# Kernel optimization log

Hardware: AMD Instinct MI355X
Metric: run time of the kernel (lower is better)

## Reference

```python
import jax, jax.numpy as jnp
import numpy as np

B, N, M = 2, 2048, 1024
C, CTX, H = 1024, 1024, 16
D = C // H
HID = int(C * 4.0)
EPS = 1e-6


def _ln(h):
    # LayerNorm32: fp32 layernorm, eps=1e-6, no affine params
    h32 = h.astype(jnp.float32)
    mu = jnp.mean(h32, axis=-1, keepdims=True)
    var = jnp.var(h32, axis=-1, keepdims=True)
    return ((h32 - mu) * jax.lax.rsqrt(var + EPS)).astype(h.dtype)


def _sdpa(q, k, v):
    # q: [B,Q,H,D], k/v: [B,K,H,D]
    scale = 1.0 / np.sqrt(D)
    s = jnp.einsum('bqhd,bkhd->bhqk', q, k) * scale
    p = jax.nn.softmax(s, axis=-1)
    return jnp.einsum('bhqk,bkhd->bqhd', p, v)


def _forward(x, context, Wqkv, bqkv, Wos, bos, Wq, bq, Wkv, bkv, Woc, boc, W1, b1, W2, b2):
    Bx, Nx, _ = x.shape
    Mx = context.shape[1]
    # --- self-attention (attn_mode='full') ---
    h = _ln(x)
    qkv = (h @ Wqkv + bqkv).reshape(Bx, Nx, 3, H, D)
    q, k, v = qkv[:, :, 0], qkv[:, :, 1], qkv[:, :, 2]
    a = _sdpa(q, k, v).reshape(Bx, Nx, C)
    x = x + (a @ Wos + bos)
    # --- cross-attention (always 'full') ---
    h = _ln(x)
    q = (h @ Wq + bq).reshape(Bx, Nx, H, D)
    kv = (context @ Wkv + bkv).reshape(Bx, Mx, 2, H, D)
    k, v = kv[:, :, 0], kv[:, :, 1]
    a = _sdpa(q, k, v).reshape(Bx, Nx, C)
    x = x + (a @ Woc + boc)
    # --- FFN with tanh-approx GELU ---
    h = _ln(x)
    x = x + (jax.nn.gelu(h @ W1 + b1, approximate=True) @ W2 + b2)
    return x


def setup_inputs() -> dict:
    key = jax.random.key(0)
    ks = jax.random.split(key, 12)
    rn = lambda k, shape: (jax.random.normal(k, shape, jnp.float32) * 0.02)
    return {
        'x': jax.random.normal(ks[0], (B, N, C), jnp.float32),
        'context': jax.random.normal(ks[1], (B, M, CTX), jnp.float32),
        'Wqkv': rn(ks[2], (C, 3 * C)), 'bqkv': jnp.zeros((3 * C,), jnp.float32),
        'Wos': rn(ks[3], (C, C)), 'bos': jnp.zeros((C,), jnp.float32),
        'Wq': rn(ks[4], (C, C)), 'bq': jnp.zeros((C,), jnp.float32),
        'Wkv': rn(ks[5], (CTX, 2 * C)), 'bkv': jnp.zeros((2 * C,), jnp.float32),
        'Woc': rn(ks[6], (C, C)), 'boc': jnp.zeros((C,), jnp.float32),
        'W1': rn(ks[7], (C, HID)), 'b1': jnp.zeros((HID,), jnp.float32),
        'W2': rn(ks[8], (HID, C)), 'b2': jnp.zeros((C,), jnp.float32),
    }


def reference(x, context, Wqkv, bqkv, Wos, bos, Wq, bq, Wkv, bkv, Woc, boc, W1, b1, W2, b2):
    return _forward(x, context, Wqkv, bqkv, Wos, bos, Wq, bq, Wkv, bkv, Woc, boc, W1, b1, W2, b2)
```

## Files before the change

kernel.cpp:

```cpp
#include <hip/hip_runtime.h>
#include <cstdint>

typedef unsigned short u16;
typedef short bf16x8 __attribute__((ext_vector_type(8)));
typedef unsigned short u16x8 __attribute__((ext_vector_type(8)));
typedef float f32x4 __attribute__((ext_vector_type(4)));

__device__ __forceinline__ u16 f2bf(float f) {
  union { float f; uint32_t u; } v; v.f = f;
  uint32_t r = (v.u + 0x7fffu + ((v.u >> 16) & 1u)) >> 16;
  return (u16)r;
}

__device__ __forceinline__ void gload_lds16(const u16* g, u16* l) {
  __builtin_amdgcn_global_load_lds(
      (const __attribute__((address_space(1))) void*)g,
      (__attribute__((address_space(3))) void*)l, 16, 0, 0);
}

__device__ __forceinline__ void ln_body(const float* __restrict__ x,
                                        u16* __restrict__ h, int row) {
  const int tid = threadIdx.x;
  const float4 v = *reinterpret_cast<const float4*>(x + (long)row * 1024 + tid * 4);
  float s  = v.x + v.y + v.z + v.w;
  float ss = v.x * v.x + v.y * v.y + v.z * v.z + v.w * v.w;
#pragma unroll
  for (int off = 32; off >= 1; off >>= 1) {
    s  += __shfl_xor(s, off, 64);
    ss += __shfl_xor(ss, off, 64);
  }
  __shared__ float red[8];
  const int wave = tid >> 6, lane = tid & 63;
  if (lane == 0) { red[wave] = s; red[4 + wave] = ss; }
  __syncthreads();
  s  = red[0] + red[1] + red[2] + red[3];
  ss = red[4] + red[5] + red[6] + red[7];
  const float mu   = s * (1.0f / 1024.0f);
  const float var  = ss * (1.0f / 1024.0f) - mu * mu;
  const float rstd = rsqrtf(var + 1e-6f);
  ushort4 o;
  o.x = f2bf((v.x - mu) * rstd);
  o.y = f2bf((v.y - mu) * rstd);
  o.z = f2bf((v.z - mu) * rstd);
  o.w = f2bf((v.w - mu) * rstd);
  *reinterpret_cast<ushort4*>(h + (long)row * 1024 + tid * 4) = o;
}

__global__ __launch_bounds__(256) void ln_kernel(const float* __restrict__ x,
                                                 u16* __restrict__ h) {
  ln_body(x, h, blockIdx.x);
}

struct WEnt { const float* W; u16* Wt; int K, N, tEnd; };
struct WEnts { WEnt e[4]; int n; };

__device__ __forceinline__ void wconv_body(const WEnts& args, int t) {
  __shared__ u16 tile[64][72];
  int i = 0, tStart = 0;
  while (i < args.n - 1 && t >= args.e[i].tEnd) { tStart = args.e[i].tEnd; i++; }
  const float* W = args.e[i].W;
  u16* Wt = args.e[i].Wt;
  const int K = args.e[i].K, N = args.e[i].N;
  const int rel = t - tStart;
  const int ntn = N >> 6;
  const int tn = rel % ntn, tk = rel / ntn;
  const int n0 = tn * 64, k0 = tk * 64;

  const int th = threadIdx.x;
  const int c4 = (th & 15) * 4;
  const int r  = th >> 4;
#pragma unroll
  for (int ii = 0; ii < 4; ii++) {
    const int row = ii * 16 + r;
    const float4 v = *reinterpret_cast<const float4*>(W + (long)(k0 + row) * N + n0 + c4);
    tile[c4 + 0][row] = f2bf(v.x);
    tile[c4 + 1][row] = f2bf(v.y);
    tile[c4 + 2][row] = f2bf(v.z);
    tile[c4 + 3][row] = f2bf(v.w);
  }
  __syncthreads();
  const int c8 = (th & 7) * 8;
  const int rn = th >> 3;
#pragma unroll
  for (int ii = 0; ii < 2; ii++) {
    const int row = ii * 32 + rn;
    *reinterpret_cast<u16x8*>(Wt + (long)(n0 + row) * K + k0 + c8) =
        *reinterpret_cast<const u16x8*>(&tile[row][c8]);
  }
}

__global__ __launch_bounds__(256) void wconvert_all(WEnts args) {
  wconv_body(args, blockIdx.x);
}

__global__ __launch_bounds__(256) void ln_wconv_combo(const float* __restrict__ x,
                                                      u16* __restrict__ h, int nLn,
                                                      WEnts args) {
  if ((int)blockIdx.x < nLn) ln_body(x, h, blockIdx.x);
  else                       wconv_body(args, blockIdx.x - nLn);
}

__global__ __launch_bounds__(256) void wconv_f2bf_combo(WEnts args, int nW,
                                                        const float* __restrict__ in,
                                                        u16* __restrict__ out) {
  if ((int)blockIdx.x < nW) {
    wconv_body(args, blockIdx.x);
  } else {
    const long i = ((long)(blockIdx.x - nW) * 256 + threadIdx.x) * 4;
    const float4 v = *reinterpret_cast<const float4*>(in + i);
    ushort4 o;
    o.x = f2bf(v.x); o.y = f2bf(v.y); o.z = f2bf(v.z); o.w = f2bf(v.w);
    *reinterpret_cast<ushort4*>(out + i) = o;
  }
}

__global__ __launch_bounds__(256) void vtrans(const u16* __restrict__ V,
                                              u16* __restrict__ Vt,
                                              int vStride, long vBatch, int nk) {
  __shared__ u16 tile[64][72];
  const int t = threadIdx.x;
  const int b = blockIdx.z, h = blockIdx.y, n0 = blockIdx.x * 64;
  const u16* vp = V + (long)b * vBatch + h * 64;
  u16* op = Vt + (long)(b * 16 + h) * 64 * (long)nk + n0;
  const int ch = t & 7;
#pragma unroll
  for (int i = 0; i < 2; i++) {
    const int n = (t >> 3) + i * 32;
    const u16x8 v = *reinterpret_cast<const u16x8*>(vp + (long)(n0 + n) * vStride + ch * 8);
#pragma unroll
    for (int j = 0; j < 8; j++) tile[ch * 8 + j][n] = v[j];
  }
  __syncthreads();
#pragma unroll
  for (int i = 0; i < 2; i++) {
    const int d = (t >> 3) + i * 32;
    *reinterpret_cast<u16x8*>(op + (long)d * nk + ch * 8) =
        *reinterpret_cast<const u16x8*>(&tile[d][ch * 8]);
  }
}

template <int TN, bool OUT_BF16, bool GELU_ACT, bool RES>
__device__ __forceinline__ void gemm_core(
    const u16* __restrict__ A, const u16* __restrict__ Bt,
    const float* __restrict__ bias, const float* __restrict__ res,
    void* __restrict__ Cout, int Ndim, int Kdim, int m0, int n0,
    u16* Al, u16* Bl) {
  constexpr int NFRAG = TN / 32;
  const int tid  = threadIdx.x;
  const int lane = tid & 63, wave = tid >> 6;
  const int quad = lane >> 4, l15 = lane & 15;
  const int wr = wave >> 1, wc = wave & 1;

  f32x4 acc[4][NFRAG];
  const f32x4 vzero = {0.f, 0.f, 0.f, 0.f};
#pragma unroll
  for (int i = 0; i < 4; i++)
#pragma unroll
    for (int jj = 0; jj < NFRAG; jj++) acc[i][jj] = vzero;

  const long rowOff = (long)(lane >> 2) * Kdim + (((lane & 3) ^ ((lane >> 3) & 3)) * 8);
  const u16* gA = A  + (long)m0 * Kdim + rowOff;
  const u16* gB = Bt + (long)n0 * Kdim + rowOff;

  auto stage = [&](int k0, int p) {
    gload_lds16(gA + (long)(wave * 16) * Kdim + k0,       Al + p * 4096 + wave * 512);
    gload_lds16(gA + (long)((wave + 4) * 16) * Kdim + k0, Al + p * 4096 + (wave + 4) * 512);
    gload_lds16(gB + (long)(wave * 16) * Kdim + k0,       Bl + p * (TN * 32) + wave * 512);
    if constexpr (TN == 128)
      gload_lds16(gB + (long)((wave + 4) * 16) * Kdim + k0, Bl + p * (TN * 32) + (wave + 4) * 512);
  };

  const int swz = (quad ^ ((l15 >> 1) & 3)) * 8;

  stage(0, 0);
  int p = 0;
  for (int k0 = 0; k0 < Kdim; k0 += 32, p ^= 1) {
    __syncthreads();
    bf16x8 af[4], bfr[NFRAG];
#pragma unroll
    for (int mt = 0; mt < 4; mt++)
      af[mt] = *reinterpret_cast<const bf16x8*>(Al + p * 4096 + (wr * 64 + mt * 16 + l15) * 32 + swz);
#pragma unroll
    for (int nt = 0; nt < NFRAG; nt++)
      bfr[nt] = *reinterpret_cast<const bf16x8*>(Bl + p * (TN * 32) + (wc * NFRAG * 16 + nt * 16 + l15) * 32 + swz);
    if (k0 + 32 < Kdim) stage(k0 + 32, p ^ 1);
#pragma unroll
    for (int mt = 0; mt < 4; mt++)
#pragma unroll
      for (int nt = 0; nt < NFRAG; nt++)
        acc[mt][nt] = __builtin_amdgcn_mfma_f32_16x16x32_bf16(af[mt], bfr[nt], acc[mt][nt], 0, 0, 0);
  }

#pragma unroll
  for (int nt = 0; nt < NFRAG; nt++) {
    const int col = n0 + wc * NFRAG * 16 + nt * 16 + l15;
    const float bv = bias[col];
#pragma unroll
    for (int mt = 0; mt < 4; mt++) {
#pragma unroll
      for (int r = 0; r < 4; r++) {
        const int row = m0 + wr * 64 + mt * 16 + quad * 4 + r;
        float y = acc[mt][nt][r] + bv;
        if (GELU_ACT) {
          const float t = 0.7978845608028654f * (y + 0.044715f * y * y * y);
          y = y / (1.0f + __builtin_amdgcn_exp2f(-2.885390081777927f * t));
        }
        if (RES) y += res[(long)row * Ndim + col];
        if (OUT_BF16)
          ((u16*)Cout)[(long)row * Ndim + col] = f2bf(y);
        else
          ((float*)Cout)[(long)row * Ndim + col] = y;
      }
    }
  }
}

template <int TN, int SX, bool OUT_BF16, bool GELU_ACT, bool RES>
__global__ __launch_bounds__(256, 2) void gemm_bt(
    const u16* __restrict__ A, const u16* __restrict__ Bt,
    const float* __restrict__ bias, const float* __restrict__ res,
    void* __restrict__ Cout, int Ndim, int Kdim, int lx, int ly) {
  __shared__ u16 Al[2 * 128 * 32];
  __shared__ u16 Bl[2 * TN * 32];
  const int j = blockIdx.x;
  const int c = j & 7, kk = j >> 3;
  const int cx = c % SX, cy = c / SX;
  const int bx = cx * lx + (kk % lx);
  const int by = cy * ly + (kk / lx);
  gemm_core<TN, OUT_BF16, GELU_ACT, RES>(
      A, Bt, bias, res, Cout, Ndim, Kdim, by * 128, bx * TN, Al, Bl);
}

struct GemmSeg {
  const u16* A; const u16* Bt; const float* bias; u16* C;
  int Ndim, Kdim, SX, lx, ly;
};
struct GemmDualP { GemmSeg s0, s1; int nBlk0; };

template <int TN>
__global__ __launch_bounds__(256, 2) void gemm_dual(GemmDualP pp) {
  __shared__ u16 Al[2 * 128 * 32];
  __shared__ u16 Bl[2 * TN * 32];
  int j = blockIdx.x;
  GemmSeg s;
  if (j < pp.nBlk0) { s = pp.s0; } else { s = pp.s1; j -= pp.nBlk0; }
  const int c = j & 7, kk = j >> 3;
  const int cx = c % s.SX, cy = c / s.SX;
  const int bx = cx * s.lx + (kk % s.lx);
  const int by = cy * s.ly + (kk / s.lx);
  gemm_core<TN, true, false, false>(
      s.A, s.Bt, s.bias, nullptr, s.C, s.Ndim, s.Kdim, by * 128, bx * TN, Al, Bl);
}

__global__ __launch_bounds__(256, 2) void attn_kernel(
    const u16* __restrict__ Q, const u16* __restrict__ K, const u16* __restrict__ Vt,
    u16* __restrict__ O, int nk, int qStride, int kStride, int oStride,
    long qBatch, long kBatch, long oBatch) {
  __shared__ u16 Kt[2][64 * 64];
  __shared__ u16 Vl[2][64 * 64];
  __shared__ u16 Pl[4][32 * 64];

  const int tid = threadIdx.x;
  const int lane = tid & 63, wave = tid >> 6;
  const int quad = lane >> 4, l15 = lane & 15;
  const int b = blockIdx.z, hh = blockIdx.y, qt = blockIdx.x;

  const u16* qp = Q + (long)b * qBatch + hh * 64;
  const u16* kp = K + (long)b * kBatch + hh * 64;
  const u16* vp = Vt + (long)(b * 16 + hh) * 64 * (long)nk;

  bf16x8 qf[2][2];
  const int qrow = qt * 128 + wave * 32 + l15;
#pragma unroll
  for (int qg = 0; qg < 2; qg++) {
    qf[qg][0] = *reinterpret_cast<const bf16x8*>(qp + (long)(qrow + qg * 16) * qStride + quad * 8);
    qf[qg][1] = *reinterpret_cast<const bf16x8*>(qp + (long)(qrow + qg * 16) * qStride + 32 + quad * 8);
  }

  const int r8 = lane >> 3;
  const int gcol = ((lane & 7) ^ r8) * 8;
  const u16* kgA = kp + (long)(wave * 8 + r8) * kStride + gcol;
  const u16* kgB = kp + (long)((wave + 4) * 8 + r8) * kStride + gcol;
  const u16* vgA = vp + (long)(wave * 8 + r8) * nk + gcol;
  const u16* vgB = vp + (long)((wave + 4) * 8 + r8) * nk + gcol;

  const int cF = (quad ^ (l15 & 7)) * 8;

  const f32x4 vzero = {0.f, 0.f, 0.f, 0.f};
  f32x4 oAcc[2][4];
  float lSt[2] = {0.f, 0.f};
#pragma unroll
  for (int qg = 0; qg < 2; qg++)
#pragma unroll
    for (int i = 0; i < 4; i++) oAcc[qg][i] = vzero;

  const float SCL = 0.18033688f;
  const int nTiles = nk >> 6;
  const long kAdv = (long)64 * kStride;

  auto stage = [&](int kt, int p) {
    gload_lds16(kgA + kt * kAdv, &Kt[p][wave * 512]);
    gload_lds16(kgB + kt * kAdv, &Kt[p][(wave + 4) * 512]);
    gload_lds16(vgA + kt * 64,   &Vl[p][wave * 512]);
    gload_lds16(vgB + kt * 64,   &Vl[p][(wave + 4) * 512]);
  };

  stage(0, 0);
  int p = 0;
  for (int kt = 0; kt < nTiles; kt++, p ^= 1) {
    __syncthreads();
    if (kt + 1 < nTiles) stage(kt + 1, p ^ 1);

    f32x4 st[2][4];
#pragma unroll
    for (int mt = 0; mt < 4; mt++) {
      const bf16x8 kf0 = *reinterpret_cast<const bf16x8*>(&Kt[p][(mt * 16 + l15) * 64 + cF]);
      const bf16x8 kf1 = *reinterpret_cast<const bf16x8*>(&Kt[p][(mt * 16 + l15) * 64 + (cF ^ 32)]);
#pragma unroll
      for (int qg = 0; qg < 2; qg++) {
        f32x4 z = vzero;
        z = __builtin_amdgcn_mfma_f32_16x16x32_bf16(kf0, qf[qg][0], z, 0, 0, 0);
        z = __builtin_amdgcn_mfma_f32_16x16x32_bf16(kf1, qf[qg][1], z, 0, 0, 0);
        st[qg][mt] = z;
      }
    }

#pragma unroll
    for (int qg = 0; qg < 2; qg++) {
      float ps = 0.f;
#pragma unroll
      for (int mt = 0; mt < 4; mt++)
#pragma unroll
        for (int r = 0; r < 4; r++) {
          const float pw = __builtin_amdgcn_exp2f(st[qg][mt][r] * SCL);
          st[qg][mt][r] = pw;
          ps += pw;
        }
      lSt[qg] += ps;
      u16* plw = &Pl[wave][(qg * 16 + l15) * 64];
#pragma unroll
      for (int mt = 0; mt < 4; mt++) {
        union { float f; uint32_t u; } a0, a1, a2, a3;
        a0.f = st[qg][mt][0]; a1.f = st[qg][mt][1];
        a2.f = st[qg][mt][2]; a3.f = st[qg][mt][3];
        a0.u += 0x8000u; a1.u += 0x8000u; a2.u += 0x8000u; a3.u += 0x8000u;
        uint2 w;
        w.x = __builtin_amdgcn_perm(a1.u, a0.u, 0x07060302u);
        w.y = __builtin_amdgcn_perm(a3.u, a2.u, 0x07060302u);
        const int pcol = (((mt * 2 + (quad >> 1)) ^ (l15 & 7)) * 8) + (quad & 1) * 4;
        *reinterpret_cast<uint2*>(&plw[pcol]) = w;
      }
    }

    bf16x8 pf[2][2];
#pragma unroll
    for (int qg = 0; qg < 2; qg++) {
      const u16* plw = &Pl[wave][(qg * 16 + l15) * 64];
      pf[qg][0] = *reinterpret_cast<const bf16x8*>(&plw[cF]);
      pf[qg][1] = *reinterpret_cast<const bf16x8*>(&plw[cF ^ 32]);
    }
#pragma unroll
    for (int dt = 0; dt < 4; dt++) {
      const bf16x8 vf0 = *reinterpret_cast<const bf16x8*>(&Vl[p][(dt * 16 + l15) * 64 + cF]);
      const bf16x8 vf1 = *reinterpret_cast<const bf16x8*>(&Vl[p][(dt * 16 + l15) * 64 + (cF ^ 32)]);
#pragma unroll
      for (int qg = 0; qg < 2; qg++) {
        oAcc[qg][dt] = __builtin_amdgcn_mfma_f32_16x16x32_bf16(pf[qg][0], vf0, oAcc[qg][dt], 0, 0, 0);
        oAcc[qg][dt] = __builtin_amdgcn_mfma_f32_16x16x32_bf16(pf[qg][1], vf1, oAcc[qg][dt], 0, 0, 0);
      }
    }
  }

  u16* op = O + (long)b * oBatch + hh * 64;
#pragma unroll
  for (int qg = 0; qg < 2; qg++) {
    float l = lSt[qg];
    l += __shfl_xor(l, 16, 64);
    l += __shfl_xor(l, 32, 64);
    float lR[4];
#pragma unroll
    for (int r = 0; r < 4; r++) lR[r] = 1.0f / __shfl(l, quad * 4 + r, 64);
#pragma unroll
    for (int dt = 0; dt < 4; dt++)
#pragma unroll
      for (int r = 0; r < 4; r++) {
        const int row = qt * 128 + wave * 32 + qg * 16 + quad * 4 + r;
        op[(long)row * oStride + dt * 16 + l15] = f2bf(oAcc[qg][dt][r] * lR[r]);
      }
  }
}

extern "C" void kernel_launch(void* const* d_in, const int* in_sizes, int n_in,
                              void* d_out, int out_size, void* d_ws, size_t ws_size,
                              hipStream_t stream) {
  const float* x    = (const float*)d_in[0];
  const float* ctx  = (const float*)d_in[1];
  const float* Wqkv = (const float*)d_in[2];
  const float* bqkv = (const float*)d_in[3];
  const float* Wos  = (const float*)d_in[4];
  const float* bos  = (const float*)d_in[5];
  const float* Wq   = (const float*)d_in[6];
  const float* bq   = (const float*)d_in[7];
  const float* Wkv  = (const float*)d_in[8];
  const float* bkv  = (const float*)d_in[9];
  const float* Woc  = (const float*)d_in[10];
  const float* boc  = (const float*)d_in[11];
  const float* W1   = (const float*)d_in[12];
  const float* b1   = (const float*)d_in[13];
  const float* W2   = (const float*)d_in[14];
  const float* b2   = (const float*)d_in[15];
  float* out = (float*)d_out;
  char* ws = (char*)d_ws;
  const size_t MB = 1024 * 1024;

  u16* h      = (u16*)ws;
  u16* abuf   = (u16*)(ws + 8 * MB);
  u16* wbuf   = (u16*)(ws + 8 * MB);
  u16* qkv    = (u16*)(ws + 16 * MB);
  u16* Wqkvt  = (u16*)(ws + 40 * MB);
  u16* Wost   = (u16*)(ws + 16 * MB);
  u16* Wqt    = (u16*)(ws + 18 * MB);
  u16* Wkvt   = (u16*)(ws + 20 * MB);
  u16* Woct   = (u16*)(ws + 24 * MB);
  u16* q2     = (u16*)(ws + 26 * MB);
  u16* kv2    = (u16*)(ws + 34 * MB);
  u16* ctxbf  = (u16*)(ws + 42 * MB);
  u16* VtCr   = (u16*)(ws + 16 * MB);
  u16* hid    = (u16*)(ws + 16 * MB);
  u16* VtSelf = h;
  u16* W1t    = wbuf;
  u16* W2t    = wbuf;

  WEnts w1; w1.n = 1;

  w1.e[0] = {Wqkv, Wqkvt, 1024, 3072, 768};
  ln_wconv_combo<<<dim3(4096 + 768), dim3(256), 0, stream>>>(x, h, 4096, w1);
  gemm_bt<128, 2, true, false, false><<<dim3(768), dim3(256), 0, stream>>>(
      h, Wqkvt, bqkv, nullptr, qkv, 3072, 1024, 12, 8);
  vtrans<<<dim3(32, 16, 2), dim3(256), 0, stream>>>(
      qkv + 2048, VtSelf, 3072, (long)2048 * 3072, 2048);
  attn_kernel<<<dim3(16, 16, 2), dim3(256), 0, stream>>>(
      qkv, qkv + 1024, VtSelf, abuf, 2048, 3072, 3072, 1024,
      (long)2048 * 3072, (long)2048 * 3072, (long)2048 * 1024);

  WEnts w4; w4.n = 4;
  w4.e[0] = {Wos, Wost, 1024, 1024, 256};
  w4.e[1] = {Wq,  Wqt,  1024, 1024, 512};
  w4.e[2] = {Wkv, Wkvt, 1024, 2048, 1024};
  w4.e[3] = {Woc, Woct, 1024, 1024, 1280};
  wconv_f2bf_combo<<<dim3(1280 + 2048), dim3(256), 0, stream>>>(w4, 1280, ctx, ctxbf);

  gemm_bt<64, 1, false, false, true><<<dim3(512), dim3(256), 0, stream>>>(
      abuf, Wost, bos, x, out, 1024, 1024, 16, 4);
  ln_kernel<<<dim3(4096), dim3(256), 0, stream>>>(out, h);

  GemmDualP dp;
  dp.s0 = {h,     Wqt,  bq,  q2,  1024, 1024, 1, 16, 4};
  dp.s1 = {ctxbf, Wkvt, bkv, kv2, 2048, 1024, 2, 16, 4};
  dp.nBlk0 = 512;
  gemm_dual<64><<<dim3(1024), dim3(256), 0, stream>>>(dp);
  vtrans<<<dim3(16, 16, 2), dim3(256), 0, stream>>>(
      kv2 + 1024, VtCr, 2048, (long)1024 * 2048, 1024);
  attn_kernel<<<dim3(16, 16, 2), dim3(256), 0, stream>>>(
      q2, kv2, VtCr, abuf, 1024, 1024, 2048, 1024,
      (long)2048 * 1024, (long)1024 * 2048, (long)2048 * 1024);
  gemm_bt<64, 1, false, false, true><<<dim3(512), dim3(256), 0, stream>>>(
      abuf, Woct, boc, out, out, 1024, 1024, 16, 4);

  w1.e[0] = {W1, W1t, 1024, 4096, 1024};
  ln_wconv_combo<<<dim3(4096 + 1024), dim3(256), 0, stream>>>(out, h, 4096, w1);
  gemm_bt<128, 2, true, true, false><<<dim3(1024), dim3(256), 0, stream>>>(
      h, W1t, b1, nullptr, hid, 4096, 1024, 16, 8);
  w1.e[0] = {W2, W2t, 4096, 1024, 1024};
  wconvert_all<<<dim3(1024), dim3(256), 0, stream>>>(w1);
  gemm_bt<64, 1, false, false, true><<<dim3(512), dim3(256), 0, stream>>>(
      hid, W2t, b2, out, out, 1024, 4096, 16, 4);
}
```

Baseline: 468.1 us.

## Double GEMM K-tile to 64 with 8-way XOR swizzle and narrower QKV/W1 tiles

```diff
diff --git a/kernel.cpp b/kernel.cpp
--- a/kernel.cpp
+++ b/kernel.cpp
@@ -145,55 +145,71 @@
     const float* __restrict__ bias, const float* __restrict__ res,
     void* __restrict__ Cout, int Ndim, int Kdim, int m0, int n0,
     u16* Al, u16* Bl) {
-  constexpr int NFRAG = TN / 32;
+  constexpr int NF = TN / 32;
+  constexpr int ABUF = 128 * 64;
+  constexpr int BBUF = TN * 64;
   const int tid  = threadIdx.x;
   const int lane = tid & 63, wave = tid >> 6;
   const int quad = lane >> 4, l15 = lane & 15;
   const int wr = wave >> 1, wc = wave & 1;
 
-  f32x4 acc[4][NFRAG];
+  f32x4 acc[4][NF];
   const f32x4 vzero = {0.f, 0.f, 0.f, 0.f};
 #pragma unroll
   for (int i = 0; i < 4; i++)
 #pragma unroll
-    for (int jj = 0; jj < NFRAG; jj++) acc[i][jj] = vzero;
-
-  const long rowOff = (long)(lane >> 2) * Kdim + (((lane & 3) ^ ((lane >> 3) & 3)) * 8);
-  const u16* gA = A  + (long)m0 * Kdim + rowOff;
-  const u16* gB = Bt + (long)n0 * Kdim + rowOff;
+    for (int jj = 0; jj < NF; jj++) acc[i][jj] = vzero;
+
+  const int srcRow = lane >> 3;
+  const int srcG   = ((lane & 7) ^ (srcRow & 7)) * 8;
+  const u16* gA = A  + (long)(m0 + srcRow) * Kdim + srcG;
+  const u16* gB = Bt + (long)(n0 + srcRow) * Kdim + srcG;
 
   auto stage = [&](int k0, int p) {
-    gload_lds16(gA + (long)(wave * 16) * Kdim + k0,       Al + p * 4096 + wave * 512);
-    gload_lds16(gA + (long)((wave + 4) * 16) * Kdim + k0, Al + p * 4096 + (wave + 4) * 512);
-    gload_lds16(gB + (long)(wave * 16) * Kdim + k0,       Bl + p * (TN * 32) + wave * 512);
-    if constexpr (TN == 128)
-      gload_lds16(gB + (long)((wave + 4) * 16) * Kdim + k0, Bl + p * (TN * 32) + (wave + 4) * 512);
+#pragma unroll
+    for (int i = 0; i < 4; i++)
+      gload_lds16(gA + (long)(wave * 32 + i * 8) * Kdim + k0,
+                  Al + p * ABUF + wave * 2048 + i * 512);
+#pragma unroll
+    for (int i = 0; i < TN / 32; i++)
+      gload_lds16(gB + (long)(wave * (TN / 4) + i * 8) * Kdim + k0,
+                  Bl + p * BBUF + wave * (TN * 16) + i * 512);
   };
 
-  const int swz = (quad ^ ((l15 >> 1) & 3)) * 8;
+  const int off0 = (quad ^ (l15 & 7)) * 8;
 
   stage(0, 0);
   int p = 0;
-  for (int k0 = 0; k0 < Kdim; k0 += 32, p ^= 1) {
+  for (int k0 = 0; k0 < Kdim; k0 += 64, p ^= 1) {
     __syncthreads();
-    bf16x8 af[4], bfr[NFRAG];
-#pragma unroll
-    for (int mt = 0; mt < 4; mt++)
-      af[mt] = *reinterpret_cast<const bf16x8*>(Al + p * 4096 + (wr * 64 + mt * 16 + l15) * 32 + swz);
-#pragma unroll
-    for (int nt = 0; nt < NFRAG; nt++)
-      bfr[nt] = *reinterpret_cast<const bf16x8*>(Bl + p * (TN * 32) + (wc * NFRAG * 16 + nt * 16 + l15) * 32 + swz);
-    if (k0 + 32 < Kdim) stage(k0 + 32, p ^ 1);
-#pragma unroll
-    for (int mt = 0; mt < 4; mt++)
-#pragma unroll
-      for (int nt = 0; nt < NFRAG; nt++)
-        acc[mt][nt] = __builtin_amdgcn_mfma_f32_16x16x32_bf16(af[mt], bfr[nt], acc[mt][nt], 0, 0, 0);
-  }
-
-#pragma unroll
-  for (int nt = 0; nt < NFRAG; nt++) {
-    const int col = n0 + wc * NFRAG * 16 + nt * 16 + l15;
+    bf16x8 af[2][4], bfr[2][NF];
+    const u16* ab = Al + p * ABUF;
+    const u16* bb = Bl + p * BBUF;
+#pragma unroll
+    for (int mt = 0; mt < 4; mt++) {
+      const int r = (wr * 64 + mt * 16 + l15) * 64;
+      af[0][mt] = *reinterpret_cast<const bf16x8*>(ab + r + off0);
+      af[1][mt] = *reinterpret_cast<const bf16x8*>(ab + r + (off0 ^ 32));
+    }
+#pragma unroll
+    for (int nt = 0; nt < NF; nt++) {
+      const int r = (wc * (NF * 16) + nt * 16 + l15) * 64;
+      bfr[0][nt] = *reinterpret_cast<const bf16x8*>(bb + r + off0);
+      bfr[1][nt] = *reinterpret_cast<const bf16x8*>(bb + r + (off0 ^ 32));
+    }
+    if (k0 + 64 < Kdim) stage(k0 + 64, p ^ 1);
+#pragma unroll
+    for (int s = 0; s < 2; s++)
+#pragma unroll
+      for (int mt = 0; mt < 4; mt++)
+#pragma unroll
+        for (int nt = 0; nt < NF; nt++)
+          acc[mt][nt] = __builtin_amdgcn_mfma_f32_16x16x32_bf16(af[s][mt], bfr[s][nt], acc[mt][nt], 0, 0, 0);
+  }
+
+#pragma unroll
+  for (int nt = 0; nt < NF; nt++) {
+    const int col = n0 + wc * (NF * 16) + nt * 16 + l15;
     const float bv = bias[col];
 #pragma unroll
     for (int mt = 0; mt < 4; mt++) {
@@ -220,8 +236,8 @@
     const u16* __restrict__ A, const u16* __restrict__ Bt,
     const float* __restrict__ bias, const float* __restrict__ res,
     void* __restrict__ Cout, int Ndim, int Kdim, int lx, int ly) {
-  __shared__ u16 Al[2 * 128 * 32];
-  __shared__ u16 Bl[2 * TN * 32];
+  __shared__ u16 Al[2 * 128 * 64];
+  __shared__ u16 Bl[2 * TN * 64];
   const int j = blockIdx.x;
   const int c = j & 7, kk = j >> 3;
   const int cx = c % SX, cy = c / SX;
@@ -239,8 +255,8 @@
 
 template <int TN>
 __global__ __launch_bounds__(256, 2) void gemm_dual(GemmDualP pp) {
-  __shared__ u16 Al[2 * 128 * 32];
-  __shared__ u16 Bl[2 * TN * 32];
+  __shared__ u16 Al[2 * 128 * 64];
+  __shared__ u16 Bl[2 * TN * 64];
   int j = blockIdx.x;
   GemmSeg s;
   if (j < pp.nBlk0) { s = pp.s0; } else { s = pp.s1; j -= pp.nBlk0; }
@@ -435,8 +451,8 @@
 
   w1.e[0] = {Wqkv, Wqkvt, 1024, 3072, 768};
   ln_wconv_combo<<<dim3(4096 + 768), dim3(256), 0, stream>>>(x, h, 4096, w1);
-  gemm_bt<128, 2, true, false, false><<<dim3(768), dim3(256), 0, stream>>>(
-      h, Wqkvt, bqkv, nullptr, qkv, 3072, 1024, 12, 8);
+  gemm_bt<64, 2, true, false, false><<<dim3(1536), dim3(256), 0, stream>>>(
+      h, Wqkvt, bqkv, nullptr, qkv, 3072, 1024, 24, 8);
   vtrans<<<dim3(32, 16, 2), dim3(256), 0, stream>>>(
       qkv + 2048, VtSelf, 3072, (long)2048 * 3072, 2048);
   attn_kernel<<<dim3(16, 16, 2), dim3(256), 0, stream>>>(
@@ -469,8 +485,8 @@
 
   w1.e[0] = {W1, W1t, 1024, 4096, 1024};
   ln_wconv_combo<<<dim3(4096 + 1024), dim3(256), 0, stream>>>(out, h, 4096, w1);
-  gemm_bt<128, 2, true, true, false><<<dim3(1024), dim3(256), 0, stream>>>(
-      h, W1t, b1, nullptr, hid, 4096, 1024, 16, 8);
+  gemm_bt<64, 2, true, true, false><<<dim3(2048), dim3(256), 0, stream>>>(
+      h, W1t, b1, nullptr, hid, 4096, 1024, 32, 8);
   w1.e[0] = {W2, W2t, 4096, 1024, 1024};
   wconvert_all<<<dim3(1024), dim3(256), 0, stream>>>(w1);
   gemm_bt<64, 1, false, false, true><<<dim3(512), dim3(256), 0, stream>>>(
```

Result: faster. 444.8 us (-5.0%).
